# Kernel tuning notes

Hardware: AMD Instinct MI355X
Metric: run time of the kernel (lower is better)

The kernel has to match this reference:

```python
import jax, jax.numpy as jnp
import numpy as np

N, NF, D, H, L, FFN, E, EF = 2048, 64, 256, 8, 6, 1024, 32768, 16
HD = D // H
MAXDEG, MAXDIST = 64, 8


def setup_inputs() -> dict:
    key = jax.random.key(0)
    ks = jax.random.split(key, 32)
    s = 0.02
    nrm = lambda k, sh: (jax.random.normal(k, sh, jnp.float32) * s)
    return {
        "x": jax.random.normal(ks[0], (N, NF), jnp.float32),
        "edge_attr": jax.random.normal(ks[1], (E, EF), jnp.float32),
        "node_proj_w": nrm(ks[2], (D, NF)),
        "node_proj_b": jnp.zeros((D,), jnp.float32),
        "in_deg_emb": nrm(ks[3], (MAXDEG + 1, D)),
        "out_deg_emb": nrm(ks[4], (MAXDEG + 1, D)),
        "dist_bias": nrm(ks[5], (MAXDIST + 2, H)),
        "edge_proj_w": nrm(ks[6], (H, EF)),
        "edge_proj_b": jnp.zeros((H,), jnp.float32),
        "cls_token": nrm(ks[7], (1, D)),
        "q_w": nrm(ks[8], (L, D, D)), "q_b": jnp.zeros((L, D)),
        "k_w": nrm(ks[9], (L, D, D)), "k_b": jnp.zeros((L, D)),
        "v_w": nrm(ks[10], (L, D, D)), "v_b": jnp.zeros((L, D)),
        "o_w": nrm(ks[11], (L, D, D)), "o_b": jnp.zeros((L, D)),
        "ffn1_w": nrm(ks[12], (L, FFN, D)), "ffn1_b": jnp.zeros((L, FFN)),
        "ffn2_w": nrm(ks[13], (L, D, FFN)), "ffn2_b": jnp.zeros((L, D)),
        "ln1_s": jnp.ones((L, D)), "ln1_b": jnp.zeros((L, D)),
        "ln2_s": jnp.ones((L, D)), "ln2_b": jnp.zeros((L, D)),
        "fn_s": jnp.ones((D,)), "fn_b": jnp.zeros((D,)),
        "edge_index": jax.random.randint(ks[14], (2, E), 0, N, dtype=jnp.int32),
        "dist_matrix": jax.random.randint(ks[15], (N, N), 0, MAXDIST + 2, dtype=jnp.int32),
    }


def _ln(v, s, b):
    m = v.mean(-1, keepdims=True)
    va = v.var(-1, keepdims=True)
    return (v - m) / jnp.sqrt(va + 1e-5) * s + b


def _forward(x, edge_attr, node_proj_w, node_proj_b, in_deg_emb, out_deg_emb,
             dist_bias, edge_proj_w, edge_proj_b, cls_token,
             q_w, q_b, k_w, k_b, v_w, v_b, o_w, o_b,
             ffn1_w, ffn1_b, ffn2_w, ffn2_b,
             ln1_s, ln1_b, ln2_s, ln2_b, fn_s, fn_b,
             edge_index, dist_matrix):
    # node embedding + degree encoding
    h = x @ node_proj_w.T + node_proj_b  # (N, D)
    ones = jnp.ones((E,), jnp.int32)
    in_deg = jnp.clip(jax.ops.segment_sum(ones, edge_index[1], num_segments=N), 0, MAXDEG)
    out_deg = jnp.clip(jax.ops.segment_sum(ones, edge_index[0], num_segments=N), 0, MAXDEG)
    h = h + in_deg_emb[in_deg] + out_deg_emb[out_deg]
    h = jnp.concatenate([cls_token, h], axis=0)  # (N+1, D), CLS at row 0
    Nf = N + 1
    # spatial bias: pad dist matrix with zeros for CLS, then embed
    dist_p = jnp.pad(jnp.clip(dist_matrix, 0, MAXDIST + 1), ((1, 0), (1, 0)))
    bias = dist_bias[dist_p]  # (Nf, Nf, H)
    # edge-feature bias: scatter-add projected edge features into dense (N,N,H)
    proj = edge_attr @ edge_proj_w.T + edge_proj_b  # (E, H)
    ebias = jnp.zeros((N, N, H), h.dtype).at[edge_index[0], edge_index[1]].add(proj)
    bias = bias + jnp.pad(ebias, ((1, 0), (1, 0), (0, 0)))
    bias_t = bias.transpose(2, 0, 1)  # (H, Nf, Nf)
    scale = np.sqrt(HD).astype(np.float32)
    for l in range(L):
        hn = _ln(h, ln1_s[l], ln1_b[l])
        Q = (hn @ q_w[l].T + q_b[l]).reshape(Nf, H, HD).transpose(1, 0, 2)
        K = (hn @ k_w[l].T + k_b[l]).reshape(Nf, H, HD).transpose(1, 0, 2)
        V = (hn @ v_w[l].T + v_b[l]).reshape(Nf, H, HD).transpose(1, 0, 2)
        logits = jnp.einsum('hnd,hmd->hnm', Q, K) / scale + bias_t
        attn = jax.nn.softmax(logits, axis=-1)
        o = jnp.einsum('hnm,hmd->hnd', attn, V).transpose(1, 0, 2).reshape(Nf, D)
        h = h + o @ o_w[l].T + o_b[l]
        hn2 = _ln(h, ln2_s[l], ln2_b[l])
        h = h + jax.nn.gelu(hn2 @ ffn1_w[l].T + ffn1_b[l], approximate=False) @ ffn2_w[l].T + ffn2_b[l]
    h = _ln(h, fn_s, fn_b)
    return h, h[0]


def reference(x, edge_attr, node_proj_w, node_proj_b, in_deg_emb, out_deg_emb,
              dist_bias, edge_proj_w, edge_proj_b, cls_token,
              q_w, q_b, k_w, k_b, v_w, v_b, o_w, o_b,
              ffn1_w, ffn1_b, ffn2_w, ffn2_b,
              ln1_s, ln1_b, ln2_s, ln2_b, fn_s, fn_b,
              edge_index, dist_matrix):
    return _forward(x, edge_attr, node_proj_w, node_proj_b, in_deg_emb, out_deg_emb,
                    dist_bias, edge_proj_w, edge_proj_b, cls_token,
                    q_w, q_b, k_w, k_b, v_w, v_b, o_w, o_b,
                    ffn1_w, ffn1_b, ffn2_w, ffn2_b,
                    ln1_s, ln1_b, ln2_s, ln2_b, fn_s, fn_b,
                    edge_index, dist_matrix)
```

## Files before the change

kernel.cpp:

```cpp
#include <hip/hip_runtime.h>
#include <math.h>

#define N_ 2048
#define NF_IN 64
#define D_ 256
#define H_ 8
#define HD_ 32
#define L_ 6
#define FFN_ 1024
#define E_ 32768
#define EF_ 16
#define NF 2049
#define MAXDEG_ 64
#define BSTRIDE 2112
#define RPAD 2112
#define NSPLIT 8

typedef __attribute__((ext_vector_type(8))) short bf16x8;
typedef __attribute__((ext_vector_type(4))) float f32x4;

__device__ inline unsigned short f2b(float f){
  union { float f; unsigned u; } v; v.f = f;
  unsigned r = (v.u + 0x7fffu + ((v.u >> 16) & 1u)) >> 16;
  return (unsigned short)r;
}
__device__ inline float b2f(short s){
  union { unsigned u; float f; } v; v.u = ((unsigned)(unsigned short)s) << 16;
  return v.f;
}

__device__ inline void atomic_add_bf16(short* p, float add){
  unsigned* wp = (unsigned*)((size_t)p & ~(size_t)3);
  bool hi = ((size_t)p & 2) != 0;
  unsigned old = *wp, assumed;
  do {
    assumed = old;
    unsigned short cur = hi ? (unsigned short)(assumed >> 16)
                            : (unsigned short)(assumed & 0xffffu);
    float f = b2f((short)cur) + add;
    unsigned short nb = f2b(f);
    unsigned nw = hi ? ((assumed & 0x0000ffffu) | ((unsigned)nb << 16))
                     : ((assumed & 0xffff0000u) | (unsigned)nb);
    old = atomicCAS(wp, assumed, nw);
  } while (old != assumed);
}

__device__ inline float wred_sum(float v){
  #pragma unroll
  for (int o = 32; o > 0; o >>= 1) v += __shfl_down(v, o, 64);
  return v;
}

__global__ void zero_int(int* p, int n){
  int i = blockIdx.x * blockDim.x + threadIdx.x;
  if (i < n) p[i] = 0;
}

__global__ void deg_count(const int* __restrict__ ei, int* __restrict__ ind,
                          int* __restrict__ outd){
  int e = blockIdx.x * blockDim.x + threadIdx.x;
  if (e >= E_) return;
  atomicAdd(&outd[ei[e]], 1);
  atomicAdd(&ind[ei[E_ + e]], 1);
}

__global__ void embed_k(const float* __restrict__ x, const float* __restrict__ W,
                        const float* __restrict__ b, const float* __restrict__ inE,
                        const float* __restrict__ outE, const int* __restrict__ ind,
                        const int* __restrict__ outd, const float* __restrict__ cls,
                        float* __restrict__ h){
  int i = blockIdx.x, d = threadIdx.x;
  if (i == 0){ h[d] = cls[d]; return; }
  int n = i - 1;
  const float4* xr = (const float4*)(x + (long)n * NF_IN);
  const float4* wr = (const float4*)(W + (long)d * NF_IN);
  float acc = b[d];
  #pragma unroll
  for (int k = 0; k < NF_IN / 4; k++){
    float4 a = xr[k], w = wr[k];
    acc += a.x * w.x + a.y * w.y + a.z * w.z + a.w * w.w;
  }
  int id = min(ind[n], MAXDEG_), od = min(outd[n], MAXDEG_);
  acc += inE[(long)id * D_ + d] + outE[(long)od * D_ + d];
  h[(long)i * D_ + d] = acc;
}

__global__ void bias_fill(const int* __restrict__ dist, const float* __restrict__ db,
                          short* __restrict__ bb){
  __shared__ float lutS[10][H_];
  int i = blockIdx.x;
  if (threadIdx.x < 80) ((float*)lutS)[threadIdx.x] = db[threadIdx.x];
  __syncthreads();
  for (int u = threadIdx.x; u < BSTRIDE / 8; u += 256){
    int dp[8];
    #pragma unroll
    for (int k = 0; k < 8; k++){
      int j = u * 8 + k;
      int d = 0;
      if (i > 0 && j > 0 && j < NF){
        int dv = dist[(long)(i - 1) * N_ + (j - 1)];
        d = max(0, min(dv, 9));
      }
      dp[k] = (j < NF) ? d : -1;
    }
    #pragma unroll
    for (int h = 0; h < H_; h++){
      short s[8];
      #pragma unroll
      for (int k = 0; k < 8; k++)
        s[k] = (dp[k] >= 0) ? (short)f2b(lutS[dp[k]][h]) : (short)0;
      *(bf16x8*)(bb + ((long)h * NF + i) * BSTRIDE + u * 8) = *(bf16x8*)s;
    }
  }
}

__global__ void edge_bias(const float* __restrict__ ea, const float* __restrict__ W,
                          const float* __restrict__ b, const int* __restrict__ ei,
                          short* __restrict__ bb){
  int e = blockIdx.x * blockDim.x + threadIdx.x;
  if (e >= E_) return;
  float a[EF_];
  #pragma unroll
  for (int k = 0; k < EF_; k++) a[k] = ea[(long)e * EF_ + k];
  int src = ei[e], dst = ei[E_ + e];
  #pragma unroll
  for (int h = 0; h < H_; h++){
    float p = b[h];
    #pragma unroll
    for (int k = 0; k < EF_; k++) p += a[k] * W[h * EF_ + k];
    atomic_add_bf16(bb + ((long)h * NF + src + 1) * BSTRIDE + (dst + 1), p);
  }
}

__global__ void w2b(const float* __restrict__ src, short* __restrict__ dst,
                    long n, long per, long ostride, long ooff){
  long i = (long)blockIdx.x * 256 + threadIdx.x;
  if (i >= n) return;
  long l = i / per, r = i - l * per;
  dst[l * ostride + ooff + r] = (short)f2b(src[i]);
}

__global__ void ln_k(const float* __restrict__ in, const float* __restrict__ s,
                     const float* __restrict__ b, float* __restrict__ outf,
                     short* __restrict__ outb, int dup0){
  __shared__ float r1[4], r2[4];
  int i = blockIdx.x, d = threadIdx.x;
  float v = in[(long)i * D_ + d];
  float s1 = wred_sum(v), s2 = wred_sum(v * v);
  if ((d & 63) == 0){ r1[d >> 6] = s1; r2[d >> 6] = s2; }
  __syncthreads();
  float S1 = r1[0] + r1[1] + r1[2] + r1[3];
  float S2 = r2[0] + r2[1] + r2[2] + r2[3];
  float m = S1 * (1.0f / D_);
  float var = S2 * (1.0f / D_) - m * m;
  float y = (v - m) * rsqrtf(var + 1e-5f) * s[d] + b[d];
  if (outf){
    outf[(long)i * D_ + d] = y;
    if (dup0 && i == 0) outf[(long)NF * D_ + d] = y;
  }
  if (outb) outb[(long)i * D_ + d] = (short)f2b(y);
}

__global__ __launch_bounds__(256) void qkv_gemm(const short* __restrict__ A,
    const short* __restrict__ Wall, const float* __restrict__ qb,
    const float* __restrict__ kb, const float* __restrict__ vb,
    short* __restrict__ QKb, short* __restrict__ Vtg, int l){
  const int z = blockIdx.z;
  const short* W = Wall + ((long)(l * 3 + z)) * D_ * D_;
  const float* bsp = (z == 0) ? qb : (z == 1) ? kb : vb;
  __shared__ __align__(16) short As[64][40], Ws[64][40];
  const int tid = threadIdx.x, lane = tid & 63, wave = tid >> 6;
  const int col = lane & 15, quad = lane >> 4;
  const int wm = wave & 1, wn = wave >> 1;
  const int bm = blockIdx.x * 64, bn = blockIdx.y * 64;
  const f32x4 zero4 = {0.f, 0.f, 0.f, 0.f};
  f32x4 acc[2][2] = {{zero4, zero4}, {zero4, zero4}};
  const int row = tid >> 2, seg = tid & 3;
  for (int k0 = 0; k0 < D_; k0 += 32){
    __syncthreads();
    bf16x8 av = (bf16x8)(short)0;
    int gm = bm + row;
    if (gm < NF) av = *(const bf16x8*)(A + (long)gm * D_ + k0 + seg * 8);
    *(bf16x8*)&As[row][seg * 8] = av;
    *(bf16x8*)&Ws[row][seg * 8] = *(const bf16x8*)(W + (long)(bn + row) * D_ + k0 + seg * 8);
    __syncthreads();
    bf16x8 a0 = *(const bf16x8*)&As[wm * 32 + col][quad * 8];
    bf16x8 a1 = *(const bf16x8*)&As[wm * 32 + 16 + col][quad * 8];
    bf16x8 b0 = *(const bf16x8*)&Ws[wn * 32 + col][quad * 8];
    bf16x8 b1 = *(const bf16x8*)&Ws[wn * 32 + 16 + col][quad * 8];
    acc[0][0] = __builtin_amdgcn_mfma_f32_16x16x32_bf16(a0, b0, acc[0][0], 0, 0, 0);
    acc[0][1] = __builtin_amdgcn_mfma_f32_16x16x32_bf16(a0, b1, acc[0][1], 0, 0, 0);
    acc[1][0] = __builtin_amdgcn_mfma_f32_16x16x32_bf16(a1, b0, acc[1][0], 0, 0, 0);
    acc[1][1] = __builtin_amdgcn_mfma_f32_16x16x32_bf16(a1, b1, acc[1][1], 0, 0, 0);
  }
  #pragma unroll
  for (int i = 0; i < 2; i++)
    #pragma unroll
    for (int j = 0; j < 2; j++)
      #pragma unroll
      for (int r = 0; r < 4; r++){
        int gm = bm + wm * 32 + i * 16 + quad * 4 + r;
        if (gm >= NF) continue;
        int gn = bn + wn * 32 + j * 16 + col;
        float v = acc[i][j][r] + bsp[gn];
        if (z < 2) QKb[(long)z * NF * D_ + (long)gm * D_ + gn] = (short)f2b(v);
        else       Vtg[(long)gn * BSTRIDE + gm] = (short)f2b(v);
      }
}

template<int ACT, int RES, int OUTF, int OUTB, int ATOM>
__global__ __launch_bounds__(256) void mgemm(const short* __restrict__ A,
    const short* __restrict__ W, const float* __restrict__ bs,
    const float* __restrict__ R, float* __restrict__ Cf, short* __restrict__ Cb,
    int M, int Nn, int Kc, int Kstride){
  __shared__ __align__(16) short As[64][40], Ws[64][40];
  const int tid = threadIdx.x, lane = tid & 63, wave = tid >> 6;
  const int col = lane & 15, quad = lane >> 4;
  const int wm = wave & 1, wn = wave >> 1;
  const int bm = blockIdx.x * 64, bn = blockIdx.y * 64;
  const int koff = blockIdx.z * Kc;
  const f32x4 zero4 = {0.f, 0.f, 0.f, 0.f};
  f32x4 acc[2][2] = {{zero4, zero4}, {zero4, zero4}};
  const int row = tid >> 2, seg = tid & 3;
  for (int k0 = 0; k0 < Kc; k0 += 32){
    __syncthreads();
    bf16x8 av = (bf16x8)(short)0;
    int gm = bm + row;
    if (gm < M) av = *(const bf16x8*)(A + (long)gm * Kstride + koff + k0 + seg * 8);
    *(bf16x8*)&As[row][seg * 8] = av;
    *(bf16x8*)&Ws[row][seg * 8] =
      *(const bf16x8*)(W + (long)(bn + row) * Kstride + koff + k0 + seg * 8);
    __syncthreads();
    bf16x8 a0 = *(const bf16x8*)&As[wm * 32 + col][quad * 8];
    bf16x8 a1 = *(const bf16x8*)&As[wm * 32 + 16 + col][quad * 8];
    bf16x8 b0 = *(const bf16x8*)&Ws[wn * 32 + col][quad * 8];
    bf16x8 b1 = *(const bf16x8*)&Ws[wn * 32 + 16 + col][quad * 8];
    acc[0][0] = __builtin_amdgcn_mfma_f32_16x16x32_bf16(a0, b0, acc[0][0], 0, 0, 0);
    acc[0][1] = __builtin_amdgcn_mfma_f32_16x16x32_bf16(a0, b1, acc[0][1], 0, 0, 0);
    acc[1][0] = __builtin_amdgcn_mfma_f32_16x16x32_bf16(a1, b0, acc[1][0], 0, 0, 0);
    acc[1][1] = __builtin_amdgcn_mfma_f32_16x16x32_bf16(a1, b1, acc[1][1], 0, 0, 0);
  }
  #pragma unroll
  for (int i = 0; i < 2; i++)
    #pragma unroll
    for (int j = 0; j < 2; j++)
      #pragma unroll
      for (int r = 0; r < 4; r++){
        int gm = bm + wm * 32 + i * 16 + quad * 4 + r;
        if (gm >= M) continue;
        int gn = bn + wn * 32 + j * 16 + col;
        if (ATOM){
          float v = acc[i][j][r] + (blockIdx.z == 0 ? bs[gn] : 0.f);
          atomicAdd(&Cf[(long)gm * Nn + gn], v);
        } else {
          float v = acc[i][j][r] + bs[gn];
          if (ACT == 1) v = v * 0.5f * (1.0f + erff(v * 0.70710678118654752f));
          if (RES) v += R[(long)gm * Nn + gn];
          if (OUTF) Cf[(long)gm * Nn + gn] = v;
          if (OUTB) Cb[(long)gm * Nn + gn] = (short)f2b(v);
        }
      }
}

__global__ __launch_bounds__(256) void fattn_k(const short* __restrict__ Qb,
    const short* __restrict__ Kb, const short* __restrict__ Vtg,
    const short* __restrict__ biasb, float* __restrict__ Opart,
    float* __restrict__ Lpart){
  __shared__ __align__(16) short Ks[64][40];
  __shared__ __align__(16) short Vt[32][72];
  __shared__ __align__(16) short PB[4][16][72];

  const int tid = threadIdx.x, wave = tid >> 6, lane = tid & 63;
  const int col = lane & 15, quad = lane >> 4;
  const int h = blockIdx.y, qz = blockIdx.z;
  const int i0b = blockIdx.x * 64;
  const int i0 = i0b + wave * 16;
  const int t0 = (qz == 0) ? 0 : 5 + 4 * (qz - 1);
  const int t1 = t0 + ((qz == 0) ? 5 : 4);

  int qrow = min(i0 + col, NF - 1);
  bf16x8 qf = *(const bf16x8*)(Qb + (long)qrow * D_ + h * HD_ + quad * 8);

  f32x4 oacc0 = {0.f, 0.f, 0.f, 0.f}, oacc1 = {0.f, 0.f, 0.f, 0.f};
  float rs[4] = {0.f, 0.f, 0.f, 0.f};
  const f32x4 zero4 = {0.f, 0.f, 0.f, 0.f};
  const float scale = 0.17677669529663687f;

  for (int t = t0; t < t1; t++){
    const int j0 = t * 64;
    __syncthreads();
    {
      int key = tid >> 2, seg = tid & 3;
      int j = j0 + key;
      bf16x8 kv = (bf16x8)(short)0;
      if (j < NF) kv = *(const bf16x8*)(Kb + (long)j * D_ + h * HD_ + seg * 8);
      *(bf16x8*)&Ks[key][seg * 8] = kv;
    }
    {
      int d = tid >> 3, seg = tid & 7;
      *(bf16x8*)&Vt[d][seg * 8] =
        *(const bf16x8*)(Vtg + (long)(h * HD_ + d) * BSTRIDE + j0 + seg * 8);
    }
    #pragma unroll
    for (int it = 0; it < 2; it++){
      int idx = it * 64 + lane;
      int rw = idx >> 3, seg = idx & 7;
      int irow = min(i0b + wave * 16 + rw, NF - 1);
      *(bf16x8*)&PB[wave][rw][seg * 8] =
        *(const bf16x8*)(biasb + ((long)h * NF + irow) * BSTRIDE + j0 + seg * 8);
    }
    __syncthreads();

    f32x4 sacc[4];
    #pragma unroll
    for (int t4 = 0; t4 < 4; t4++){
      bf16x8 kf = *(const bf16x8*)&Ks[t4 * 16 + col][quad * 8];
      sacc[t4] = __builtin_amdgcn_mfma_f32_16x16x32_bf16(qf, kf, zero4, 0, 0, 0);
    }

    const bool tail = (j0 + 64 > NF);
    #pragma unroll
    for (int r = 0; r < 4; r++){
      #pragma unroll
      for (int t4 = 0; t4 < 4; t4++){
        float bv = b2f(PB[wave][quad * 4 + r][t4 * 16 + col]);
        float p = __expf(sacc[t4][r] * scale + bv);
        if (tail && (j0 + t4 * 16 + col >= NF)) p = 0.f;
        rs[r] += p;
        PB[wave][quad * 4 + r][t4 * 16 + col] = (short)f2b(p);
      }
    }

    #pragma unroll
    for (int ks = 0; ks < 2; ks++){
      bf16x8 af = *(const bf16x8*)&PB[wave][col][ks * 32 + quad * 8];
      bf16x8 v0 = *(const bf16x8*)&Vt[col][ks * 32 + quad * 8];
      bf16x8 v1 = *(const bf16x8*)&Vt[16 + col][ks * 32 + quad * 8];
      oacc0 = __builtin_amdgcn_mfma_f32_16x16x32_bf16(af, v0, oacc0, 0, 0, 0);
      oacc1 = __builtin_amdgcn_mfma_f32_16x16x32_bf16(af, v1, oacc1, 0, 0, 0);
    }
  }

  #pragma unroll
  for (int r = 0; r < 4; r++){
    #pragma unroll
    for (int o = 1; o < 16; o <<= 1) rs[r] += __shfl_xor(rs[r], o, 64);
  }
  long pi = ((long)qz * H_ + h) * RPAD + i0 + quad * 4;
  #pragma unroll
  for (int r = 0; r < 4; r++){
    Opart[(pi + r) * HD_ + col] = oacc0[r];
    Opart[(pi + r) * HD_ + 16 + col] = oacc1[r];
    if (col == 0) Lpart[pi + r] = rs[r];
  }
}

__global__ void attn_merge(const float* __restrict__ Op, const float* __restrict__ Lp,
                           short* __restrict__ omb){
  int i = blockIdx.x;
  int h = threadIdx.x >> 5, d = threadIdx.x & 31;
  float s = 0.f, o = 0.f;
  #pragma unroll
  for (int q = 0; q < NSPLIT; q++){
    long pi = ((long)q * H_ + h) * RPAD + i;
    s += Lp[pi];
    o += Op[pi * HD_ + d];
  }
  omb[(long)i * D_ + h * HD_ + d] = (short)f2b(o / s);
}

extern "C" void kernel_launch(void* const* d_in, const int* in_sizes, int n_in,
                              void* d_out, int out_size, void* d_ws, size_t ws_size,
                              hipStream_t stream){
  const float* x    = (const float*)d_in[0];
  const float* ea   = (const float*)d_in[1];
  const float* npw  = (const float*)d_in[2];
  const float* npb  = (const float*)d_in[3];
  const float* inE  = (const float*)d_in[4];
  const float* outE = (const float*)d_in[5];
  const float* db   = (const float*)d_in[6];
  const float* epw  = (const float*)d_in[7];
  const float* epb  = (const float*)d_in[8];
  const float* cls  = (const float*)d_in[9];
  const float* qw   = (const float*)d_in[10];
  const float* qb   = (const float*)d_in[11];
  const float* kw   = (const float*)d_in[12];
  const float* kb   = (const float*)d_in[13];
  const float* vw   = (const float*)d_in[14];
  const float* vb   = (const float*)d_in[15];
  const float* ow   = (const float*)d_in[16];
  const float* ob   = (const float*)d_in[17];
  const float* f1w  = (const float*)d_in[18];
  const float* f1b  = (const float*)d_in[19];
  const float* f2w  = (const float*)d_in[20];
  const float* f2bp = (const float*)d_in[21];
  const float* ln1s = (const float*)d_in[22];
  const float* ln1b = (const float*)d_in[23];
  const float* ln2s = (const float*)d_in[24];
  const float* ln2b = (const float*)d_in[25];
  const float* fns  = (const float*)d_in[26];
  const float* fnb  = (const float*)d_in[27];
  const int*   ei   = (const int*)d_in[28];
  const int*   dist = (const int*)d_in[29];

  float* ws = (float*)d_ws;
  long off = 0;
  float* h     = ws + off; off += (long)NF * D_;
  float* Opart = ws + off; off += (long)NSPLIT * H_ * RPAD * HD_;
  float* Lpart = ws + off; off += (long)NSPLIT * H_ * RPAD;
  short* biasb = (short*)(ws + off); off += ((long)H_ * NF * BSTRIDE + 1) / 2;
  short* hnb   = (short*)(ws + off); off += ((long)NF * D_ + 1) / 2;
  short* QKb   = (short*)(ws + off); off += (long)NF * D_;
  short* Vtg   = (short*)(ws + off); off += ((long)D_ * BSTRIDE + 1) / 2;
  short* omb   = (short*)(ws + off); off += ((long)NF * D_ + 1) / 2;
  short* midb  = (short*)(ws + off); off += ((long)NF * FFN_ + 1) / 2;
  short* wqkv  = (short*)(ws + off); off += ((long)3 * L_ * D_ * D_ + 1) / 2;
  short* owb   = (short*)(ws + off); off += ((long)L_ * D_ * D_ + 1) / 2;
  short* f1wb  = (short*)(ws + off); off += ((long)L_ * FFN_ * D_ + 1) / 2;
  short* f2wb  = (short*)(ws + off); off += ((long)L_ * FFN_ * D_ + 1) / 2;
  int*   ind   = (int*)(ws + off);
  int*   outd  = ind + N_;

  zero_int<<<(2 * N_ + 255) / 256, 256, 0, stream>>>(ind, 2 * N_);
  deg_count<<<(E_ + 255) / 256, 256, 0, stream>>>(ei, ind, outd);
  embed_k<<<NF, D_, 0, stream>>>(x, npw, npb, inE, outE, ind, outd, cls, h);
  bias_fill<<<NF, 256, 0, stream>>>(dist, db, biasb);
  edge_bias<<<(E_ + 255) / 256, 256, 0, stream>>>(ea, epw, epb, ei, biasb);

  {
    long nw = (long)L_ * D_ * D_;
    int gb = (int)((nw + 255) / 256);
    w2b<<<gb, 256, 0, stream>>>(qw, wqkv, nw, (long)D_ * D_, (long)3 * D_ * D_, 0);
    w2b<<<gb, 256, 0, stream>>>(kw, wqkv, nw, (long)D_ * D_, (long)3 * D_ * D_, (long)D_ * D_);
    w2b<<<gb, 256, 0, stream>>>(vw, wqkv, nw, (long)D_ * D_, (long)3 * D_ * D_, (long)2 * D_ * D_);
    w2b<<<gb, 256, 0, stream>>>(ow, owb, nw, nw, 0, 0);
    long nf = (long)L_ * FFN_ * D_;
    int gf = (int)((nf + 255) / 256);
    w2b<<<gf, 256, 0, stream>>>(f1w, f1wb, nf, nf, 0, 0);
    w2b<<<gf, 256, 0, stream>>>(f2w, f2wb, nf, nf, 0, 0);
  }

  dim3 gQKV((NF + 63) / 64, D_ / 64, 3);
  dim3 gO((NF + 63) / 64, D_ / 64, 2);
  dim3 gF((NF + 63) / 64, FFN_ / 64, 1);
  dim3 gF2((NF + 63) / 64, D_ / 64, 4);
  dim3 gA((NF + 63) / 64, H_, NSPLIT);
  for (int l = 0; l < L_; l++){
    ln_k<<<NF, D_, 0, stream>>>(h, ln1s + l * D_, ln1b + l * D_, nullptr, hnb, 0);
    qkv_gemm<<<gQKV, 256, 0, stream>>>(hnb, wqkv, qb + l * D_, kb + l * D_, vb + l * D_,
                                       QKb, Vtg, l);
    fattn_k<<<gA, 256, 0, stream>>>(QKb, QKb + (long)NF * D_, Vtg, biasb, Opart, Lpart);
    attn_merge<<<NF, 256, 0, stream>>>(Opart, Lpart, omb);
    mgemm<0,0,0,0,1><<<gO, 256, 0, stream>>>(omb, owb + (long)l * D_ * D_, ob + l * D_,
                                             nullptr, h, nullptr, NF, D_, 128, D_);
    ln_k<<<NF, D_, 0, stream>>>(h, ln2s + l * D_, ln2b + l * D_, nullptr, hnb, 0);
    mgemm<1,0,0,1,0><<<gF, 256, 0, stream>>>(hnb, f1wb + (long)l * FFN_ * D_, f1b + l * FFN_,
                                             nullptr, nullptr, midb, NF, FFN_, D_, D_);
    mgemm<0,0,0,0,1><<<gF2, 256, 0, stream>>>(midb, f2wb + (long)l * FFN_ * D_, f2bp + l * D_,
                                              nullptr, h, nullptr, NF, D_, 256, FFN_);
  }
  ln_k<<<NF, D_, 0, stream>>>(h, fns, fnb, (float*)d_out, nullptr, 1);
}
```

Measured before the change: 695.6 us.

## Fuse attention split merge into atomics and O-proj GEMM, widen GEMM K-tile

The attention kernel now atomically adds its partial outputs and row sums into one shared buffer, which is zeroed each layer with a memset. This removes the separate merge kernel and its eight-way partial buffers. The O-projection GEMM reads those fp32 partials, normalizes them and converts to bf16 while loading its A tile, so the intermediate bf16 buffer is no longer needed. The attention kernel also reads bias directly from global memory instead of staging it in LDS, and the GEMMs step through K in 64-wide chunks to halve the number of barriers. The cost is more atomic traffic, non-deterministic summation order, and uncoalesced bias reads in the attention kernel.

Result: slower. 808.5 us (+16.2%).

```diff
diff --git a/kernel.cpp b/kernel.cpp
--- a/kernel.cpp
+++ b/kernel.cpp
@@ -168,7 +168,7 @@
   const int z = blockIdx.z;
   const short* W = Wall + ((long)(l * 3 + z)) * D_ * D_;
   const float* bsp = (z == 0) ? qb : (z == 1) ? kb : vb;
-  __shared__ __align__(16) short As[64][40], Ws[64][40];
+  __shared__ __align__(16) short As[64][72], Ws[64][72];
   const int tid = threadIdx.x, lane = tid & 63, wave = tid >> 6;
   const int col = lane & 15, quad = lane >> 4;
   const int wm = wave & 1, wn = wave >> 1;
@@ -176,22 +176,32 @@
   const f32x4 zero4 = {0.f, 0.f, 0.f, 0.f};
   f32x4 acc[2][2] = {{zero4, zero4}, {zero4, zero4}};
   const int row = tid >> 2, seg = tid & 3;
-  for (int k0 = 0; k0 < D_; k0 += 32){
-    __syncthreads();
-    bf16x8 av = (bf16x8)(short)0;
+  for (int k0 = 0; k0 < D_; k0 += 64){
+    __syncthreads();
     int gm = bm + row;
-    if (gm < NF) av = *(const bf16x8*)(A + (long)gm * D_ + k0 + seg * 8);
-    *(bf16x8*)&As[row][seg * 8] = av;
-    *(bf16x8*)&Ws[row][seg * 8] = *(const bf16x8*)(W + (long)(bn + row) * D_ + k0 + seg * 8);
-    __syncthreads();
-    bf16x8 a0 = *(const bf16x8*)&As[wm * 32 + col][quad * 8];
-    bf16x8 a1 = *(const bf16x8*)&As[wm * 32 + 16 + col][quad * 8];
-    bf16x8 b0 = *(const bf16x8*)&Ws[wn * 32 + col][quad * 8];
-    bf16x8 b1 = *(const bf16x8*)&Ws[wn * 32 + 16 + col][quad * 8];
-    acc[0][0] = __builtin_amdgcn_mfma_f32_16x16x32_bf16(a0, b0, acc[0][0], 0, 0, 0);
-    acc[0][1] = __builtin_amdgcn_mfma_f32_16x16x32_bf16(a0, b1, acc[0][1], 0, 0, 0);
-    acc[1][0] = __builtin_amdgcn_mfma_f32_16x16x32_bf16(a1, b0, acc[1][0], 0, 0, 0);
-    acc[1][1] = __builtin_amdgcn_mfma_f32_16x16x32_bf16(a1, b1, acc[1][1], 0, 0, 0);
+    bf16x8 av0 = (bf16x8)(short)0, av1 = (bf16x8)(short)0;
+    if (gm < NF){
+      const short* ar = A + (long)gm * D_ + k0 + seg * 8;
+      av0 = *(const bf16x8*)ar;
+      av1 = *(const bf16x8*)(ar + 32);
+    }
+    *(bf16x8*)&As[row][seg * 8] = av0;
+    *(bf16x8*)&As[row][seg * 8 + 32] = av1;
+    const short* wr = W + (long)(bn + row) * D_ + k0 + seg * 8;
+    *(bf16x8*)&Ws[row][seg * 8] = *(const bf16x8*)wr;
+    *(bf16x8*)&Ws[row][seg * 8 + 32] = *(const bf16x8*)(wr + 32);
+    __syncthreads();
+    #pragma unroll
+    for (int ks = 0; ks < 2; ks++){
+      bf16x8 a0 = *(const bf16x8*)&As[wm * 32 + col][ks * 32 + quad * 8];
+      bf16x8 a1 = *(const bf16x8*)&As[wm * 32 + 16 + col][ks * 32 + quad * 8];
+      bf16x8 b0 = *(const bf16x8*)&Ws[wn * 32 + col][ks * 32 + quad * 8];
+      bf16x8 b1 = *(const bf16x8*)&Ws[wn * 32 + 16 + col][ks * 32 + quad * 8];
+      acc[0][0] = __builtin_amdgcn_mfma_f32_16x16x32_bf16(a0, b0, acc[0][0], 0, 0, 0);
+      acc[0][1] = __builtin_amdgcn_mfma_f32_16x16x32_bf16(a0, b1, acc[0][1], 0, 0, 0);
+      acc[1][0] = __builtin_amdgcn_mfma_f32_16x16x32_bf16(a1, b0, acc[1][0], 0, 0, 0);
+      acc[1][1] = __builtin_amdgcn_mfma_f32_16x16x32_bf16(a1, b1, acc[1][1], 0, 0, 0);
+    }
   }
   #pragma unroll
   for (int i = 0; i < 2; i++)
@@ -208,12 +218,13 @@
       }
 }
 
-template<int ACT, int RES, int OUTF, int OUTB, int ATOM>
+template<int ACT, int ATOM, int MERGE>
 __global__ __launch_bounds__(256) void mgemm(const short* __restrict__ A,
+    const float* __restrict__ Op, const float* __restrict__ Lp,
     const short* __restrict__ W, const float* __restrict__ bs,
-    const float* __restrict__ R, float* __restrict__ Cf, short* __restrict__ Cb,
+    float* __restrict__ Cf, short* __restrict__ Cb,
     int M, int Nn, int Kc, int Kstride){
-  __shared__ __align__(16) short As[64][40], Ws[64][40];
+  __shared__ __align__(16) short As[64][72], Ws[64][72];
   const int tid = threadIdx.x, lane = tid & 63, wave = tid >> 6;
   const int col = lane & 15, quad = lane >> 4;
   const int wm = wave & 1, wn = wave >> 1;
@@ -222,23 +233,55 @@
   const f32x4 zero4 = {0.f, 0.f, 0.f, 0.f};
   f32x4 acc[2][2] = {{zero4, zero4}, {zero4, zero4}};
   const int row = tid >> 2, seg = tid & 3;
-  for (int k0 = 0; k0 < Kc; k0 += 32){
-    __syncthreads();
-    bf16x8 av = (bf16x8)(short)0;
+  for (int k0 = 0; k0 < Kc; k0 += 64){
+    __syncthreads();
     int gm = bm + row;
-    if (gm < M) av = *(const bf16x8*)(A + (long)gm * Kstride + koff + k0 + seg * 8);
-    *(bf16x8*)&As[row][seg * 8] = av;
-    *(bf16x8*)&Ws[row][seg * 8] =
-      *(const bf16x8*)(W + (long)(bn + row) * Kstride + koff + k0 + seg * 8);
-    __syncthreads();
-    bf16x8 a0 = *(const bf16x8*)&As[wm * 32 + col][quad * 8];
-    bf16x8 a1 = *(const bf16x8*)&As[wm * 32 + 16 + col][quad * 8];
-    bf16x8 b0 = *(const bf16x8*)&Ws[wn * 32 + col][quad * 8];
-    bf16x8 b1 = *(const bf16x8*)&Ws[wn * 32 + 16 + col][quad * 8];
-    acc[0][0] = __builtin_amdgcn_mfma_f32_16x16x32_bf16(a0, b0, acc[0][0], 0, 0, 0);
-    acc[0][1] = __builtin_amdgcn_mfma_f32_16x16x32_bf16(a0, b1, acc[0][1], 0, 0, 0);
-    acc[1][0] = __builtin_amdgcn_mfma_f32_16x16x32_bf16(a1, b0, acc[1][0], 0, 0, 0);
-    acc[1][1] = __builtin_amdgcn_mfma_f32_16x16x32_bf16(a1, b1, acc[1][1], 0, 0, 0);
+    if (MERGE){
+      #pragma unroll
+      for (int gI = 0; gI < 2; gI++){
+        int kg = koff + k0 + gI * 32 + seg * 8;
+        short s[8];
+        if (gm < M){
+          int hh = kg >> 5, d0 = kg & 31;
+          long base = ((long)hh * RPAD + gm) * HD_ + d0;
+          float4 v0 = *(const float4*)(Op + base);
+          float4 v1 = *(const float4*)(Op + base + 4);
+          float inv = 1.0f / Lp[(long)hh * RPAD + gm];
+          s[0] = (short)f2b(v0.x * inv); s[1] = (short)f2b(v0.y * inv);
+          s[2] = (short)f2b(v0.z * inv); s[3] = (short)f2b(v0.w * inv);
+          s[4] = (short)f2b(v1.x * inv); s[5] = (short)f2b(v1.y * inv);
+          s[6] = (short)f2b(v1.z * inv); s[7] = (short)f2b(v1.w * inv);
+        } else {
+          #pragma unroll
+          for (int k = 0; k < 8; k++) s[k] = 0;
+        }
+        *(bf16x8*)&As[row][gI * 32 + seg * 8] = *(bf16x8*)s;
+      }
+    } else {
+      bf16x8 av0 = (bf16x8)(short)0, av1 = (bf16x8)(short)0;
+      if (gm < M){
+        const short* ar = A + (long)gm * Kstride + koff + k0 + seg * 8;
+        av0 = *(const bf16x8*)ar;
+        av1 = *(const bf16x8*)(ar + 32);
+      }
+      *(bf16x8*)&As[row][seg * 8] = av0;
+      *(bf16x8*)&As[row][seg * 8 + 32] = av1;
+    }
+    const short* wr = W + (long)(bn + row) * Kstride + koff + k0 + seg * 8;
+    *(bf16x8*)&Ws[row][seg * 8] = *(const bf16x8*)wr;
+    *(bf16x8*)&Ws[row][seg * 8 + 32] = *(const bf16x8*)(wr + 32);
+    __syncthreads();
+    #pragma unroll
+    for (int ks = 0; ks < 2; ks++){
+      bf16x8 a0 = *(const bf16x8*)&As[wm * 32 + col][ks * 32 + quad * 8];
+      bf16x8 a1 = *(const bf16x8*)&As[wm * 32 + 16 + col][ks * 32 + quad * 8];
+      bf16x8 b0 = *(const bf16x8*)&Ws[wn * 32 + col][ks * 32 + quad * 8];
+      bf16x8 b1 = *(const bf16x8*)&Ws[wn * 32 + 16 + col][ks * 32 + quad * 8];
+      acc[0][0] = __builtin_amdgcn_mfma_f32_16x16x32_bf16(a0, b0, acc[0][0], 0, 0, 0);
+      acc[0][1] = __builtin_amdgcn_mfma_f32_16x16x32_bf16(a0, b1, acc[0][1], 0, 0, 0);
+      acc[1][0] = __builtin_amdgcn_mfma_f32_16x16x32_bf16(a1, b0, acc[1][0], 0, 0, 0);
+      acc[1][1] = __builtin_amdgcn_mfma_f32_16x16x32_bf16(a1, b1, acc[1][1], 0, 0, 0);
+    }
   }
   #pragma unroll
   for (int i = 0; i < 2; i++)
@@ -249,37 +292,42 @@
         int gm = bm + wm * 32 + i * 16 + quad * 4 + r;
         if (gm >= M) continue;
         int gn = bn + wn * 32 + j * 16 + col;
+        float v = acc[i][j][r];
         if (ATOM){
-          float v = acc[i][j][r] + (blockIdx.z == 0 ? bs[gn] : 0.f);
+          if (blockIdx.z == 0) v += bs[gn];
           atomicAdd(&Cf[(long)gm * Nn + gn], v);
         } else {
-          float v = acc[i][j][r] + bs[gn];
+          v += bs[gn];
           if (ACT == 1) v = v * 0.5f * (1.0f + erff(v * 0.70710678118654752f));
-          if (RES) v += R[(long)gm * Nn + gn];
-          if (OUTF) Cf[(long)gm * Nn + gn] = v;
-          if (OUTB) Cb[(long)gm * Nn + gn] = (short)f2b(v);
+          Cb[(long)gm * Nn + gn] = (short)f2b(v);
         }
       }
 }
 
 __global__ __launch_bounds__(256) void fattn_k(const short* __restrict__ Qb,
     const short* __restrict__ Kb, const short* __restrict__ Vtg,
-    const short* __restrict__ biasb, float* __restrict__ Opart,
-    float* __restrict__ Lpart){
+    const short* __restrict__ biasb, float* __restrict__ Opartm,
+    float* __restrict__ Lpartm){
   __shared__ __align__(16) short Ks[64][40];
   __shared__ __align__(16) short Vt[32][72];
-  __shared__ __align__(16) short PB[4][16][72];
+  __shared__ __align__(16) short Ps[4][16][72];
 
   const int tid = threadIdx.x, wave = tid >> 6, lane = tid & 63;
   const int col = lane & 15, quad = lane >> 4;
   const int h = blockIdx.y, qz = blockIdx.z;
-  const int i0b = blockIdx.x * 64;
-  const int i0 = i0b + wave * 16;
+  const int i0 = blockIdx.x * 64 + wave * 16;
   const int t0 = (qz == 0) ? 0 : 5 + 4 * (qz - 1);
   const int t1 = t0 + ((qz == 0) ? 5 : 4);
 
   int qrow = min(i0 + col, NF - 1);
   bf16x8 qf = *(const bf16x8*)(Qb + (long)qrow * D_ + h * HD_ + quad * 8);
+
+  const unsigned short* br[4];
+  #pragma unroll
+  for (int r = 0; r < 4; r++){
+    int ig = min(i0 + quad * 4 + r, NF - 1);
+    br[r] = (const unsigned short*)biasb + ((long)h * NF + ig) * BSTRIDE;
+  }
 
   f32x4 oacc0 = {0.f, 0.f, 0.f, 0.f}, oacc1 = {0.f, 0.f, 0.f, 0.f};
   float rs[4] = {0.f, 0.f, 0.f, 0.f};
@@ -301,14 +349,6 @@
       *(bf16x8*)&Vt[d][seg * 8] =
         *(const bf16x8*)(Vtg + (long)(h * HD_ + d) * BSTRIDE + j0 + seg * 8);
     }
-    #pragma unroll
-    for (int it = 0; it < 2; it++){
-      int idx = it * 64 + lane;
-      int rw = idx >> 3, seg = idx & 7;
-      int irow = min(i0b + wave * 16 + rw, NF - 1);
-      *(bf16x8*)&PB[wave][rw][seg * 8] =
-        *(const bf16x8*)(biasb + ((long)h * NF + irow) * BSTRIDE + j0 + seg * 8);
-    }
     __syncthreads();
 
     f32x4 sacc[4];
@@ -323,17 +363,18 @@
     for (int r = 0; r < 4; r++){
       #pragma unroll
       for (int t4 = 0; t4 < 4; t4++){
-        float bv = b2f(PB[wave][quad * 4 + r][t4 * 16 + col]);
+        float bv = b2f((short)br[r][j0 + t4 * 16 + col]);
         float p = __expf(sacc[t4][r] * scale + bv);
         if (tail && (j0 + t4 * 16 + col >= NF)) p = 0.f;
-        rs[r] += p;
-        PB[wave][quad * 4 + r][t4 * 16 + col] = (short)f2b(p);
+        short pb = (short)(__float_as_uint(p) >> 16);
+        rs[r] += b2f(pb);
+        Ps[wave][quad * 4 + r][t4 * 16 + col] = pb;
       }
     }
 
     #pragma unroll
     for (int ks = 0; ks < 2; ks++){
-      bf16x8 af = *(const bf16x8*)&PB[wave][col][ks * 32 + quad * 8];
+      bf16x8 af = *(const bf16x8*)&Ps[wave][col][ks * 32 + quad * 8];
       bf16x8 v0 = *(const bf16x8*)&Vt[col][ks * 32 + quad * 8];
       bf16x8 v1 = *(const bf16x8*)&Vt[16 + col][ks * 32 + quad * 8];
       oacc0 = __builtin_amdgcn_mfma_f32_16x16x32_bf16(af, v0, oacc0, 0, 0, 0);
@@ -346,27 +387,14 @@
     #pragma unroll
     for (int o = 1; o < 16; o <<= 1) rs[r] += __shfl_xor(rs[r], o, 64);
   }
-  long pi = ((long)qz * H_ + h) * RPAD + i0 + quad * 4;
   #pragma unroll
   for (int r = 0; r < 4; r++){
-    Opart[(pi + r) * HD_ + col] = oacc0[r];
-    Opart[(pi + r) * HD_ + 16 + col] = oacc1[r];
-    if (col == 0) Lpart[pi + r] = rs[r];
-  }
-}
-
-__global__ void attn_merge(const float* __restrict__ Op, const float* __restrict__ Lp,
-                           short* __restrict__ omb){
-  int i = blockIdx.x;
-  int h = threadIdx.x >> 5, d = threadIdx.x & 31;
-  float s = 0.f, o = 0.f;
-  #pragma unroll
-  for (int q = 0; q < NSPLIT; q++){
-    long pi = ((long)q * H_ + h) * RPAD + i;
-    s += Lp[pi];
-    o += Op[pi * HD_ + d];
-  }
-  omb[(long)i * D_ + h * HD_ + d] = (short)f2b(o / s);
+    int ig = i0 + quad * 4 + r;
+    long base = ((long)h * RPAD + ig) * HD_;
+    atomicAdd(&Opartm[base + col], oacc0[r]);
+    atomicAdd(&Opartm[base + 16 + col], oacc1[r]);
+    if (col == 0) atomicAdd(&Lpartm[(long)h * RPAD + ig], rs[r]);
+  }
 }
 
 extern "C" void kernel_launch(void* const* d_in, const int* in_sizes, int n_in,
@@ -405,21 +433,20 @@
 
   float* ws = (float*)d_ws;
   long off = 0;
-  float* h     = ws + off; off += (long)NF * D_;
-  float* Opart = ws + off; off += (long)NSPLIT * H_ * RPAD * HD_;
-  float* Lpart = ws + off; off += (long)NSPLIT * H_ * RPAD;
-  short* biasb = (short*)(ws + off); off += ((long)H_ * NF * BSTRIDE + 1) / 2;
-  short* hnb   = (short*)(ws + off); off += ((long)NF * D_ + 1) / 2;
-  short* QKb   = (short*)(ws + off); off += (long)NF * D_;
-  short* Vtg   = (short*)(ws + off); off += ((long)D_ * BSTRIDE + 1) / 2;
-  short* omb   = (short*)(ws + off); off += ((long)NF * D_ + 1) / 2;
-  short* midb  = (short*)(ws + off); off += ((long)NF * FFN_ + 1) / 2;
-  short* wqkv  = (short*)(ws + off); off += ((long)3 * L_ * D_ * D_ + 1) / 2;
-  short* owb   = (short*)(ws + off); off += ((long)L_ * D_ * D_ + 1) / 2;
-  short* f1wb  = (short*)(ws + off); off += ((long)L_ * FFN_ * D_ + 1) / 2;
-  short* f2wb  = (short*)(ws + off); off += ((long)L_ * FFN_ * D_ + 1) / 2;
-  int*   ind   = (int*)(ws + off);
-  int*   outd  = ind + N_;
+  float* h      = ws + off; off += (long)NF * D_;
+  float* Opartm = ws + off; off += (long)H_ * RPAD * HD_;
+  float* Lpartm = ws + off; off += (long)H_ * RPAD;
+  short* biasb  = (short*)(ws + off); off += ((long)H_ * NF * BSTRIDE + 1) / 2;
+  short* hnb    = (short*)(ws + off); off += ((long)NF * D_ + 1) / 2;
+  short* QKb    = (short*)(ws + off); off += (long)NF * D_;
+  short* Vtg    = (short*)(ws + off); off += ((long)D_ * BSTRIDE + 1) / 2;
+  short* midb   = (short*)(ws + off); off += ((long)NF * FFN_ + 1) / 2;
+  short* wqkv   = (short*)(ws + off); off += ((long)3 * L_ * D_ * D_ + 1) / 2;
+  short* owb    = (short*)(ws + off); off += ((long)L_ * D_ * D_ + 1) / 2;
+  short* f1wb   = (short*)(ws + off); off += ((long)L_ * FFN_ * D_ + 1) / 2;
+  short* f2wb   = (short*)(ws + off); off += ((long)L_ * FFN_ * D_ + 1) / 2;
+  int*   ind    = (int*)(ws + off);
+  int*   outd   = ind + N_;
 
   zero_int<<<(2 * N_ + 255) / 256, 256, 0, stream>>>(ind, 2 * N_);
   deg_count<<<(E_ + 255) / 256, 256, 0, stream>>>(ei, ind, outd);
@@ -440,6 +467,7 @@
     w2b<<<gf, 256, 0, stream>>>(f2w, f2wb, nf, nf, 0, 0);
   }
 
+  const size_t partBytes = (size_t)H_ * RPAD * (HD_ + 1) * sizeof(float);
   dim3 gQKV((NF + 63) / 64, D_ / 64, 3);
   dim3 gO((NF + 63) / 64, D_ / 64, 2);
   dim3 gF((NF + 63) / 64, FFN_ / 64, 1);
@@ -449,15 +477,19 @@
     ln_k<<<NF, D_, 0, stream>>>(h, ln1s + l * D_, ln1b + l * D_, nullptr, hnb, 0);
     qkv_gemm<<<gQKV, 256, 0, stream>>>(hnb, wqkv, qb + l * D_, kb + l * D_, vb + l * D_,
                                        QKb, Vtg, l);
-    fattn_k<<<gA, 256, 0, stream>>>(QKb, QKb + (long)NF * D_, Vtg, biasb, Opart, Lpart);
-    attn_merge<<<NF, 256, 0, stream>>>(Opart, Lpart, omb);
-    mgemm<0,0,0,0,1><<<gO, 256, 0, stream>>>(omb, owb + (long)l * D_ * D_, ob + l * D_,
-                                             nullptr, h, nullptr, NF, D_, 128, D_);
+    hipMemsetAsync(Opartm, 0, partBytes, stream);
+    fattn_k<<<gA, 256, 0, stream>>>(QKb, QKb + (long)NF * D_, Vtg, biasb,
+                                    Opartm, Lpartm);
+    mgemm<0,1,1><<<gO, 256, 0, stream>>>(nullptr, Opartm, Lpartm,
+                                         owb + (long)l * D_ * D_, ob + l * D_,
+                                         h, nullptr, NF, D_, 128, D_);
     ln_k<<<NF, D_, 0, stream>>>(h, ln2s + l * D_, ln2b + l * D_, nullptr, hnb, 0);
-    mgemm<1,0,0,1,0><<<gF, 256, 0, stream>>>(hnb, f1wb + (long)l * FFN_ * D_, f1b + l * FFN_,
-                                             nullptr, nullptr, midb, NF, FFN_, D_, D_);
-    mgemm<0,0,0,0,1><<<gF2, 256, 0, stream>>>(midb, f2wb + (long)l * FFN_ * D_, f2bp + l * D_,
-                                              nullptr, h, nullptr, NF, D_, 256, FFN_);
+    mgemm<1,0,0><<<gF, 256, 0, stream>>>(hnb, nullptr, nullptr,
+                                         f1wb + (long)l * FFN_ * D_, f1b + l * FFN_,
+                                         nullptr, midb, NF, FFN_, D_, D_);
+    mgemm<0,1,0><<<gF2, 256, 0, stream>>>(midb, nullptr, nullptr,
+                                          f2wb + (long)l * FFN_ * D_, f2bp + l * D_,
+                                          h, nullptr, NF, D_, 256, FFN_);
   }
   ln_k<<<NF, D_, 0, stream>>>(h, fns, fnb, (float*)d_out, nullptr, 1);
 }
```
